# Kernel optimization log

Hardware: AMD Instinct MI355X
Metric: run time of the kernel (lower is better)

Reference implementation:

```python
import jax, jax.numpy as jnp
import numpy as np

H = 128
M = 50000
L = 400000
EPS = 1e-9


def setup_inputs() -> dict:
    key = jax.random.key(0)
    ks = jax.random.split(key, 24)
    d = {
        'x_emb': jax.random.normal(ks[0], (M, H), jnp.float32),
        'child_h': jax.random.normal(ks[1], (M, H), jnp.float32),
        'child_c': jax.random.normal(ks[2], (M, H), jnp.float32),
        'pair_cand_idx': jax.random.randint(ks[3], (L,), 0, M, jnp.int32),
        'pair_child_idx': jax.random.randint(ks[4], (L,), 0, M, jnp.int32),
    }
    s = 1.0 / np.sqrt(H)
    names = ['Wi_w', 'Ui_w', 'Wf_w', 'Uf_w', 'Wo_w', 'Uo_w', 'Wc_w', 'Uc_w', 'Wa_w', 'Ua_w']
    for i, n in enumerate(names):
        d[n] = jax.random.uniform(ks[5 + i], (H, H), jnp.float32, -s, s)
    for i, n in enumerate(['Wi_b', 'Wf_b', 'Wo_b', 'Wc_b', 'Wa_b']):
        d[n] = jax.random.uniform(ks[15 + i], (H,), jnp.float32, -s, s)
    d['v_w'] = jax.random.uniform(ks[20], (H,), jnp.float32, -s, s)
    return d


def reference(x_emb, child_h, child_c, pair_cand_idx, pair_child_idx,
              Wi_w, Ui_w, Wf_w, Uf_w, Wo_w, Uo_w, Wc_w, Uc_w, Wa_w, Ua_w,
              Wi_b, Wf_b, Wo_b, Wc_b, Wa_b, v_w):
    m = x_emb.shape[0]
    ci, chi = pair_cand_idx, pair_child_idx

    # --- segment attention (torch version runs under no_grad) ---
    Ah = child_h @ Wa_w.T + Wa_b          # [M,H]
    Bx = x_emb @ Ua_w.T                   # [M,H]
    e = jnp.tanh(Ah[chi] + Bx[ci]) @ v_w  # [L]
    seg_max = jax.ops.segment_max(e, ci, num_segments=m)
    x_exp = jnp.exp(e - seg_max[ci])
    seg_sum = jax.ops.segment_sum(x_exp, ci, num_segments=m) + EPS
    attn = x_exp / seg_sum[ci]            # [L]
    h_hat = jax.ops.segment_sum(attn[:, None] * child_h[chi], ci, num_segments=m)  # [M,H]

    # --- tree-LSTM gates ---
    i_j = jax.nn.sigmoid(x_emb @ Wi_w.T + Wi_b + h_hat @ Ui_w.T)
    Wfx = x_emb @ Wf_w.T + Wf_b
    Ufh = child_h @ Uf_w.T
    f_pair = jax.nn.sigmoid(Wfx[ci] + Ufh[chi])                       # [L,H]
    sum_f_c = jax.ops.segment_sum(f_pair * child_c[chi], ci, num_segments=m)
    c_t = jnp.tanh(x_emb @ Wc_w.T + Wc_b + h_hat @ Uc_w.T)
    c = i_j * c_t + sum_f_c
    o_j = jax.nn.sigmoid(x_emb @ Wo_w.T + Wo_b + h_hat @ Uo_w.T)
    h = o_j * jnp.tanh(c)
    return (h, c)
```

## Files before the change

### kernel.cpp

```cpp
#include <hip/hip_runtime.h>
#include <cstdint>
#include <cstddef>

#define H 128
#define PSTRIDE 512

typedef __bf16 v8bf __attribute__((ext_vector_type(8)));
typedef __bf16 v4bf __attribute__((ext_vector_type(4)));
typedef float  v4f  __attribute__((ext_vector_type(4)));

__device__ __forceinline__ float ftanh(float x) {
    return 1.f - 2.f / (1.f + __expf(2.f * x));
}
__device__ __forceinline__ float fsigm(float x) {
    return 1.f / (1.f + __expf(-x));
}

struct MatDesc {
    const __bf16* A;
    int           lda;
    const __bf16* Wb;
    const float*  bias;
    __bf16*       C;
    int           ldc;
};
struct MatBatch { MatDesc m[7]; };
struct WPtrs { const float* w[10]; };

__global__ __launch_bounds__(256) void prep_k(WPtrs wp, __bf16* __restrict__ Wb,
                                              const float* __restrict__ x,
                                              const float* __restrict__ chh,
                                              const float* __restrict__ chc,
                                              __bf16* __restrict__ xe,
                                              __bf16* __restrict__ P,
                                              const int* __restrict__ ci,
                                              int* __restrict__ counts,
                                              int MH4, int L) {
    int tid = blockIdx.x * 256 + threadIdx.x;
    if (tid < 40960) {
        int mat = tid >> 12;
        int off = (tid & 4095) << 2;
        v4f a = *(const v4f*)(wp.w[mat] + off);
        v4bf b;
#pragma unroll
        for (int k = 0; k < 4; ++k) b[k] = (__bf16)a[k];
        *(v4bf*)(Wb + mat * 16384 + off) = b;
        return;
    }
    int i = tid - 40960;
    if (i < MH4) {
        v4f a = ((const v4f*)x)[i];
        v4f b = ((const v4f*)chh)[i];
        v4f c = ((const v4f*)chc)[i];
        v4bf ab, bb, cb;
#pragma unroll
        for (int k = 0; k < 4; ++k) {
            ab[k] = (__bf16)a[k]; bb[k] = (__bf16)b[k]; cb[k] = (__bf16)c[k];
        }
        ((v4bf*)xe)[i] = ab;
        int m = i >> 5;
        int q = (i & 31) << 2;
        __bf16* prow = P + (size_t)m * PSTRIDE + q;
        *(v4bf*)prow = bb;
        *(v4bf*)(prow + H) = cb;
        return;
    }
    int l = i - MH4;
    if (l < L) atomicAdd(&counts[ci[l]], 1);
}

__global__ __launch_bounds__(256) void gemm_batch(MatBatch batch, int M) {
    const MatDesc d = batch.m[blockIdx.y];
    __shared__ __bf16 wlds[H][H + 8];

    for (int t = threadIdx.x; t < 2048; t += 256) {
        int n = t >> 4;
        int k = (t & 15) << 3;
        *(v8bf*)&wlds[n][k] = *(const v8bf*)(d.Wb + n * H + k);
    }
    __syncthreads();

    const int wave = threadIdx.x >> 6;
    const int lane = threadIdx.x & 63;
    const int quad = lane >> 4;
    const int l16  = lane & 15;
    const int r0   = blockIdx.x * 128 + wave * 32;

    v4f acc0[8], acc1[8];
#pragma unroll
    for (int nt = 0; nt < 8; ++nt) {
        acc0[nt] = (v4f){0.f, 0.f, 0.f, 0.f};
        acc1[nt] = (v4f){0.f, 0.f, 0.f, 0.f};
    }

    const __bf16* ar0 = d.A + (size_t)(r0 + l16) * d.lda + quad * 8;
    const __bf16* ar1 = d.A + (size_t)(r0 + 16 + l16) * d.lda + quad * 8;
#pragma unroll
    for (int k0 = 0; k0 < H; k0 += 32) {
        v8bf a0 = *(const v8bf*)(ar0 + k0);
        v8bf a1 = *(const v8bf*)(ar1 + k0);
#pragma unroll
        for (int nt = 0; nt < 8; ++nt) {
            v8bf b = *(const v8bf*)(&wlds[nt * 16 + l16][k0 + quad * 8]);
            acc0[nt] = __builtin_amdgcn_mfma_f32_16x16x32_bf16(a0, b, acc0[nt], 0, 0, 0);
            acc1[nt] = __builtin_amdgcn_mfma_f32_16x16x32_bf16(a1, b, acc1[nt], 0, 0, 0);
        }
    }

#pragma unroll
    for (int nt = 0; nt < 8; ++nt) {
        int n = nt * 16 + l16;
        float bia = d.bias ? d.bias[n] : 0.f;
#pragma unroll
        for (int r = 0; r < 4; ++r) {
            int m0 = r0 + quad * 4 + r;
            int m1 = m0 + 16;
            if (m0 < M) d.C[(size_t)m0 * d.ldc + n] = (__bf16)(acc0[nt][r] + bia);
            if (m1 < M) d.C[(size_t)m1 * d.ldc + n] = (__bf16)(acc1[nt][r] + bia);
        }
    }
}

__global__ __launch_bounds__(1024) void scan_local(const int* __restrict__ counts,
                                                   int* __restrict__ excl,
                                                   int* __restrict__ bsums, int M) {
    __shared__ int s[1024];
    int tid = threadIdx.x;
    int idx = blockIdx.x * 1024 + tid;
    int v = (idx < M) ? counts[idx] : 0;
    s[tid] = v;
    __syncthreads();
    for (int off = 1; off < 1024; off <<= 1) {
        int t = (tid >= off) ? s[tid - off] : 0;
        __syncthreads();
        s[tid] += t;
        __syncthreads();
    }
    if (idx < M) excl[idx] = s[tid] - v;
    if (tid == 1023) bsums[blockIdx.x] = s[1023];
}

__global__ __launch_bounds__(1024) void scan_fused(int* __restrict__ rowptr,
                                                   int* __restrict__ cursor,
                                                   const int* __restrict__ bsums,
                                                   const int* __restrict__ counts,
                                                   int M, int nb) {
    __shared__ int s[1024];
    int t = threadIdx.x, b = blockIdx.x;
    int v = (t < nb) ? bsums[t] : 0;
    s[t] = v;
    __syncthreads();
    for (int off = 1; off < 1024; off <<= 1) {
        int tt = (t >= off) ? s[t - off] : 0;
        __syncthreads();
        s[t] += tt;
        __syncthreads();
    }
    int boff = (b == 0) ? 0 : s[b - 1];
    int idx = b * 1024 + t;
    if (idx < M) {
        int val = rowptr[idx] + boff;
        rowptr[idx] = val;
        cursor[idx] = val;
        if (idx == M - 1) rowptr[M] = val + counts[M - 1];
    }
}

__global__ __launch_bounds__(256) void scatter_k(const int* __restrict__ ci,
                                                 const int* __restrict__ chi,
                                                 int* __restrict__ cursor,
                                                 int* __restrict__ payload, int L) {
    int l = blockIdx.x * 256 + threadIdx.x;
    if (l < L) {
        int pos = atomicAdd(&cursor[ci[l]], 1);
        payload[pos] = chi[l];
    }
}

__global__ __launch_bounds__(128) void segment_fused(const int* __restrict__ rowptr,
                                                     const int* __restrict__ payload,
                                                     const float* __restrict__ vw,
                                                     const __bf16* __restrict__ Bx,
                                                     const __bf16* __restrict__ Wfx,
                                                     const __bf16* __restrict__ P,
                                                     __bf16* __restrict__ hhat,
                                                     float* __restrict__ sumfc, int M) {
    const int wl   = threadIdx.x & 63;
    const int half = wl & 32;
    const int l32  = wl & 31;
    const int m = blockIdx.x * 4 + (threadIdx.x >> 5);
    if (m >= M) return;
    const int start = rowptr[m];
    const int deg   = rowptr[m + 1] - start;
    const int h = l32 << 2;

    v4bf bx4 = *(const v4bf*)(Bx + (size_t)m * H + h);
    v4bf wf4 = *(const v4bf*)(Wfx + (size_t)m * H + h);
    v4f  vv  = *(const v4f*)(vw + h);
    float bxf[4], wff[4];
#pragma unroll
    for (int k = 0; k < 4; ++k) { bxf[k] = (float)bx4[k]; wff[k] = (float)wf4[k]; }

    int pl0 = (l32 < deg) ? payload[start + l32] : 0;
    int pl1 = (32 + l32 < deg) ? payload[start + 32 + l32] : 0;

    float denom = 0.f;
    float acch[4] = {0.f, 0.f, 0.f, 0.f};
    float accf[4] = {0.f, 0.f, 0.f, 0.f};

    const int jcap = deg < 64 ? deg : 64;
    for (int j = 0; j < jcap; ++j) {
        int cj = __shfl((j & 32) ? pl1 : pl0, half | (j & 31), 64);
        const __bf16* pb = P + (size_t)cj * PSTRIDE + h;
        v4bf h4 = *(const v4bf*)pb;
        v4bf c4 = *(const v4bf*)(pb + H);
        v4bf u4 = *(const v4bf*)(pb + 2 * H);
        v4bf a4 = *(const v4bf*)(pb + 3 * H);
        float s = 0.f;
#pragma unroll
        for (int k = 0; k < 4; ++k) s += ftanh((float)a4[k] + bxf[k]) * vv[k];
        s += __shfl_xor(s, 1);
        s += __shfl_xor(s, 2);
        s += __shfl_xor(s, 4);
        s += __shfl_xor(s, 8);
        s += __shfl_xor(s, 16);
        float ex = __expf(s);
        denom += ex;
#pragma unroll
        for (int k = 0; k < 4; ++k) {
            acch[k] += ex * (float)h4[k];
            accf[k] += fsigm(wff[k] + (float)u4[k]) * (float)c4[k];
        }
    }
    for (int j = 64; j < deg; ++j) {
        int cj = payload[start + j];
        const __bf16* pb = P + (size_t)cj * PSTRIDE + h;
        v4bf h4 = *(const v4bf*)pb;
        v4bf c4 = *(const v4bf*)(pb + H);
        v4bf u4 = *(const v4bf*)(pb + 2 * H);
        v4bf a4 = *(const v4bf*)(pb + 3 * H);
        float s = 0.f;
#pragma unroll
        for (int k = 0; k < 4; ++k) s += ftanh((float)a4[k] + bxf[k]) * vv[k];
        s += __shfl_xor(s, 1);
        s += __shfl_xor(s, 2);
        s += __shfl_xor(s, 4);
        s += __shfl_xor(s, 8);
        s += __shfl_xor(s, 16);
        float ex = __expf(s);
        denom += ex;
#pragma unroll
        for (int k = 0; k < 4; ++k) {
            acch[k] += ex * (float)h4[k];
            accf[k] += fsigm(wff[k] + (float)u4[k]) * (float)c4[k];
        }
    }

    float inv = 1.f / (denom + 1e-9f);
    v4bf hb;
    v4f sf;
#pragma unroll
    for (int k = 0; k < 4; ++k) { hb[k] = (__bf16)(acch[k] * inv); sf[k] = accf[k]; }
    *(v4bf*)(hhat + (size_t)m * H + h) = hb;
    *(v4f*)(sumfc + (size_t)m * H + h) = sf;
}

__global__ __launch_bounds__(256) void final_k(const __bf16* __restrict__ Xi, const __bf16* __restrict__ Hi,
                                               const __bf16* __restrict__ Xc, const __bf16* __restrict__ Hc,
                                               const __bf16* __restrict__ Xo, const __bf16* __restrict__ Ho,
                                               const float* __restrict__ sumfc,
                                               float* __restrict__ out, int MH4, int MH) {
    int i = blockIdx.x * 256 + threadIdx.x;
    if (i >= MH4) return;
    v4bf xi = ((const v4bf*)Xi)[i], hi = ((const v4bf*)Hi)[i];
    v4bf xc = ((const v4bf*)Xc)[i], hc = ((const v4bf*)Hc)[i];
    v4bf xo = ((const v4bf*)Xo)[i], ho = ((const v4bf*)Ho)[i];
    v4f sf = ((const v4f*)sumfc)[i];
    v4f hout, cout;
#pragma unroll
    for (int k = 0; k < 4; ++k) {
        float ig = fsigm((float)xi[k] + (float)hi[k]);
        float ct = ftanh((float)xc[k] + (float)hc[k]);
        float og = fsigm((float)xo[k] + (float)ho[k]);
        float c = ig * ct + sf[k];
        cout[k] = c;
        hout[k] = og * ftanh(c);
    }
    ((v4f*)out)[i] = hout;
    ((v4f*)(out + MH))[i] = cout;
}

extern "C" void kernel_launch(void* const* d_in, const int* in_sizes, int n_in,
                              void* d_out, int out_size, void* d_ws, size_t ws_size,
                              hipStream_t stream) {
    const float* x_emb   = (const float*)d_in[0];
    const float* child_h = (const float*)d_in[1];
    const float* child_c = (const float*)d_in[2];
    const int*   ci      = (const int*)d_in[3];
    const int*   chi     = (const int*)d_in[4];
    const float* Wi_b = (const float*)d_in[15];
    const float* Wf_b = (const float*)d_in[16];
    const float* Wo_b = (const float*)d_in[17];
    const float* Wc_b = (const float*)d_in[18];
    const float* Wa_b = (const float*)d_in[19];
    const float* vw   = (const float*)d_in[20];

    const int M    = in_sizes[0] / H;
    const int L    = in_sizes[3];
    const int Mpad = (M + 127) & ~127;
    const int MH   = M * H;
    const int MH4  = MH / 4;

    char* p = (char*)d_ws;
    auto alloc = [&](size_t bytes) {
        char* r = p;
        p += (bytes + 255) & ~(size_t)255;
        return (void*)r;
    };
    size_t bfbytes = (size_t)Mpad * H * sizeof(__bf16);
    __bf16* xe16   = (__bf16*)alloc(bfbytes);
    __bf16* P      = (__bf16*)alloc((size_t)Mpad * PSTRIDE * sizeof(__bf16));
    __bf16* hhat16 = (__bf16*)alloc(bfbytes);
    __bf16* Bx16   = (__bf16*)alloc(bfbytes);
    __bf16* Wfx16  = (__bf16*)alloc(bfbytes);
    __bf16* Xi16   = (__bf16*)alloc(bfbytes);
    __bf16* Xc16   = (__bf16*)alloc(bfbytes);
    __bf16* Xo16   = (__bf16*)alloc(bfbytes);
    __bf16* Wb     = (__bf16*)alloc(10 * 16384 * sizeof(__bf16));
    float* sumfc   = (float*)alloc((size_t)MH * 4);
    int*   payload = (int*)alloc((size_t)L * 4);
    int*   counts  = (int*)alloc((size_t)M * 4);
    int*   rowptr  = (int*)alloc((size_t)(M + 1) * 4);
    int*   cursor  = (int*)alloc((size_t)M * 4);
    int*   bsums   = (int*)alloc(1024 * 4);
    __bf16* Hi16 = Bx16;
    __bf16* Hc16 = Wfx16;
    __bf16* Ho16 = P;

    hipMemsetAsync(counts, 0, (size_t)M * 4, stream);

    WPtrs wp;
    for (int k = 0; k < 10; ++k) wp.w[k] = (const float*)d_in[5 + k];
    int prep_items = 40960 + MH4 + L;
    prep_k<<<(prep_items + 255) / 256, 256, 0, stream>>>(wp, Wb, x_emb, child_h, child_c,
                                                         xe16, P, ci, counts, MH4, L);

    const __bf16* Wi = Wb + 0 * 16384;
    const __bf16* Ui = Wb + 1 * 16384;
    const __bf16* Wf = Wb + 2 * 16384;
    const __bf16* Uf = Wb + 3 * 16384;
    const __bf16* Wo = Wb + 4 * 16384;
    const __bf16* Uo = Wb + 5 * 16384;
    const __bf16* Wc = Wb + 6 * 16384;
    const __bf16* Uc = Wb + 7 * 16384;
    const __bf16* Wa = Wb + 8 * 16384;
    const __bf16* Ua = Wb + 9 * 16384;

    MatBatch ba{};
    ba.m[0] = MatDesc{P,    PSTRIDE, Wa, Wa_b,    P + 3 * H, PSTRIDE};
    ba.m[1] = MatDesc{xe16, H,       Ua, nullptr, Bx16,      H};
    ba.m[2] = MatDesc{xe16, H,       Wf, Wf_b,    Wfx16,     H};
    ba.m[3] = MatDesc{P,    PSTRIDE, Uf, nullptr, P + 2 * H, PSTRIDE};
    ba.m[4] = MatDesc{xe16, H,       Wi, Wi_b,    Xi16,      H};
    ba.m[5] = MatDesc{xe16, H,       Wc, Wc_b,    Xc16,      H};
    ba.m[6] = MatDesc{xe16, H,       Wo, Wo_b,    Xo16,      H};
    dim3 gA(Mpad / 128, 7);
    gemm_batch<<<gA, 256, 0, stream>>>(ba, M);

    int nb = (M + 1023) / 1024;
    scan_local<<<nb, 1024, 0, stream>>>(counts, rowptr, bsums, M);
    scan_fused<<<nb, 1024, 0, stream>>>(rowptr, cursor, bsums, counts, M, nb);

    scatter_k<<<(L + 255) / 256, 256, 0, stream>>>(ci, chi, cursor, payload, L);

    segment_fused<<<(M + 3) / 4, 128, 0, stream>>>(rowptr, payload, vw, Bx16, Wfx16, P,
                                                   hhat16, sumfc, M);

    MatBatch bb{};
    bb.m[0] = MatDesc{hhat16, H, Ui, nullptr, Hi16, H};
    bb.m[1] = MatDesc{hhat16, H, Uc, nullptr, Hc16, H};
    bb.m[2] = MatDesc{hhat16, H, Uo, nullptr, Ho16, H};
    dim3 gB(Mpad / 128, 3);
    gemm_batch<<<gB, 256, 0, stream>>>(bb, M);

    final_k<<<(MH4 + 255) / 256, 256, 0, stream>>>(Xi16, Hi16, Xc16, Hc16, Xo16, Ho16, sumfc,
                                                   (float*)d_out, MH4, MH);
}
```

Measured before the change: 397.9 us.

## Fuse GEMMs by shared input, precompute edge scores, fuse final GEMM with gates

The x_emb GEMMs now run as one multi-stage block that converts fp32 rows to bf16 in registers once and reuses them across five weight matrices. The same kernel handles the two P-based GEMMs, and the separate bf16 copy of x_emb is dropped. A new per-edge kernel computes the exp attention scores, scatter carries them into CSR order, and the segment kernel no longer does tanh and reductions per edge. The U-projections of h_hat are fused with the gate epilogue, removing intermediate bf16 buffers and a separate elementwise pass. The costs are extra L-sized buffers, serial weight reloads with more block syncs, and a softmax that skips max subtraction.

Measured after the change: 479.5 us. +20.5%, slower.

```diff
diff --git a/kernel.cpp b/kernel.cpp
--- a/kernel.cpp
+++ b/kernel.cpp
@@ -16,22 +16,14 @@
     return 1.f / (1.f + __expf(-x));
 }
 
-struct MatDesc {
-    const __bf16* A;
-    int           lda;
-    const __bf16* Wb;
-    const float*  bias;
-    __bf16*       C;
-    int           ldc;
-};
-struct MatBatch { MatDesc m[7]; };
+struct Stage { const __bf16* W; const float* bias; __bf16* C; int ldc; };
+struct MultiDesc { const void* A; int lda; int af32; int ns; Stage st[5]; };
+struct MultiBatch { MultiDesc g[2]; };
 struct WPtrs { const float* w[10]; };
 
 __global__ __launch_bounds__(256) void prep_k(WPtrs wp, __bf16* __restrict__ Wb,
-                                              const float* __restrict__ x,
                                               const float* __restrict__ chh,
                                               const float* __restrict__ chc,
-                                              __bf16* __restrict__ xe,
                                               __bf16* __restrict__ P,
                                               const int* __restrict__ ci,
                                               int* __restrict__ counts,
@@ -49,15 +41,11 @@
     }
     int i = tid - 40960;
     if (i < MH4) {
-        v4f a = ((const v4f*)x)[i];
         v4f b = ((const v4f*)chh)[i];
         v4f c = ((const v4f*)chc)[i];
-        v4bf ab, bb, cb;
-#pragma unroll
-        for (int k = 0; k < 4; ++k) {
-            ab[k] = (__bf16)a[k]; bb[k] = (__bf16)b[k]; cb[k] = (__bf16)c[k];
-        }
-        ((v4bf*)xe)[i] = ab;
+        v4bf bb, cb;
+#pragma unroll
+        for (int k = 0; k < 4; ++k) { bb[k] = (__bf16)b[k]; cb[k] = (__bf16)c[k]; }
         int m = i >> 5;
         int q = (i & 31) << 2;
         __bf16* prow = P + (size_t)m * PSTRIDE + q;
@@ -69,16 +57,9 @@
     if (l < L) atomicAdd(&counts[ci[l]], 1);
 }
 
-__global__ __launch_bounds__(256) void gemm_batch(MatBatch batch, int M) {
-    const MatDesc d = batch.m[blockIdx.y];
+__global__ __launch_bounds__(256) void gemm_multi(MultiBatch mb, int M) {
+    const MultiDesc d = mb.g[blockIdx.y];
     __shared__ __bf16 wlds[H][H + 8];
-
-    for (int t = threadIdx.x; t < 2048; t += 256) {
-        int n = t >> 4;
-        int k = (t & 15) << 3;
-        *(v8bf*)&wlds[n][k] = *(const v8bf*)(d.Wb + n * H + k);
-    }
-    __syncthreads();
 
     const int wave = threadIdx.x >> 6;
     const int lane = threadIdx.x & 63;
@@ -86,39 +67,108 @@
     const int l16  = lane & 15;
     const int r0   = blockIdx.x * 128 + wave * 32;
 
-    v4f acc0[8], acc1[8];
-#pragma unroll
-    for (int nt = 0; nt < 8; ++nt) {
-        acc0[nt] = (v4f){0.f, 0.f, 0.f, 0.f};
-        acc1[nt] = (v4f){0.f, 0.f, 0.f, 0.f};
-    }
-
-    const __bf16* ar0 = d.A + (size_t)(r0 + l16) * d.lda + quad * 8;
-    const __bf16* ar1 = d.A + (size_t)(r0 + 16 + l16) * d.lda + quad * 8;
-#pragma unroll
-    for (int k0 = 0; k0 < H; k0 += 32) {
-        v8bf a0 = *(const v8bf*)(ar0 + k0);
-        v8bf a1 = *(const v8bf*)(ar1 + k0);
+    int ra = r0 + l16;      if (ra > M - 1) ra = M - 1;
+    int rb = r0 + 16 + l16; if (rb > M - 1) rb = M - 1;
+
+    v8bf a0[4], a1[4];
+    if (d.af32) {
+        const float* A = (const float*)d.A;
+        const float* p0 = A + (size_t)ra * d.lda + quad * 8;
+        const float* p1 = A + (size_t)rb * d.lda + quad * 8;
+#pragma unroll
+        for (int k0 = 0; k0 < 4; ++k0) {
+            v4f x0a = *(const v4f*)(p0 + k0 * 32);
+            v4f x0b = *(const v4f*)(p0 + k0 * 32 + 4);
+            v4f x1a = *(const v4f*)(p1 + k0 * 32);
+            v4f x1b = *(const v4f*)(p1 + k0 * 32 + 4);
+            v8bf t0, t1;
+#pragma unroll
+            for (int k = 0; k < 4; ++k) {
+                t0[k] = (__bf16)x0a[k]; t0[k + 4] = (__bf16)x0b[k];
+                t1[k] = (__bf16)x1a[k]; t1[k + 4] = (__bf16)x1b[k];
+            }
+            a0[k0] = t0; a1[k0] = t1;
+        }
+    } else {
+        const __bf16* A = (const __bf16*)d.A;
+        const __bf16* p0 = A + (size_t)ra * d.lda + quad * 8;
+        const __bf16* p1 = A + (size_t)rb * d.lda + quad * 8;
+#pragma unroll
+        for (int k0 = 0; k0 < 4; ++k0) {
+            a0[k0] = *(const v8bf*)(p0 + k0 * 32);
+            a1[k0] = *(const v8bf*)(p1 + k0 * 32);
+        }
+    }
+
+    for (int s = 0; s < d.ns; ++s) {
+        if (s) __syncthreads();
+        for (int t = threadIdx.x; t < 2048; t += 256) {
+            int n = t >> 4;
+            int k = (t & 15) << 3;
+            *(v8bf*)&wlds[n][k] = *(const v8bf*)(d.st[s].W + n * H + k);
+        }
+        __syncthreads();
+
+        v4f acc0[8], acc1[8];
 #pragma unroll
         for (int nt = 0; nt < 8; ++nt) {
-            v8bf b = *(const v8bf*)(&wlds[nt * 16 + l16][k0 + quad * 8]);
-            acc0[nt] = __builtin_amdgcn_mfma_f32_16x16x32_bf16(a0, b, acc0[nt], 0, 0, 0);
-            acc1[nt] = __builtin_amdgcn_mfma_f32_16x16x32_bf16(a1, b, acc1[nt], 0, 0, 0);
-        }
-    }
-
-#pragma unroll
-    for (int nt = 0; nt < 8; ++nt) {
-        int n = nt * 16 + l16;
-        float bia = d.bias ? d.bias[n] : 0.f;
-#pragma unroll
-        for (int r = 0; r < 4; ++r) {
-            int m0 = r0 + quad * 4 + r;
-            int m1 = m0 + 16;
-            if (m0 < M) d.C[(size_t)m0 * d.ldc + n] = (__bf16)(acc0[nt][r] + bia);
-            if (m1 < M) d.C[(size_t)m1 * d.ldc + n] = (__bf16)(acc1[nt][r] + bia);
-        }
-    }
+            acc0[nt] = (v4f){0.f, 0.f, 0.f, 0.f};
+            acc1[nt] = (v4f){0.f, 0.f, 0.f, 0.f};
+        }
+#pragma unroll
+        for (int k0 = 0; k0 < 4; ++k0) {
+#pragma unroll
+            for (int nt = 0; nt < 8; ++nt) {
+                v8bf b = *(const v8bf*)(&wlds[nt * 16 + l16][k0 * 32 + quad * 8]);
+                acc0[nt] = __builtin_amdgcn_mfma_f32_16x16x32_bf16(a0[k0], b, acc0[nt], 0, 0, 0);
+                acc1[nt] = __builtin_amdgcn_mfma_f32_16x16x32_bf16(a1[k0], b, acc1[nt], 0, 0, 0);
+            }
+        }
+
+        const float* bias = d.st[s].bias;
+        __bf16* C = d.st[s].C;
+        const int ldc = d.st[s].ldc;
+#pragma unroll
+        for (int nt = 0; nt < 8; ++nt) {
+            int n = nt * 16 + l16;
+            float bia = bias ? bias[n] : 0.f;
+#pragma unroll
+            for (int r = 0; r < 4; ++r) {
+                int m0 = r0 + quad * 4 + r;
+                int m1 = m0 + 16;
+                if (m0 < M) C[(size_t)m0 * ldc + n] = (__bf16)(acc0[nt][r] + bia);
+                if (m1 < M) C[(size_t)m1 * ldc + n] = (__bf16)(acc1[nt][r] + bia);
+            }
+        }
+    }
+}
+
+__global__ __launch_bounds__(256) void edge_score(const int* __restrict__ ci,
+                                                  const int* __restrict__ chi,
+                                                  const float* __restrict__ vw,
+                                                  const __bf16* __restrict__ Bx,
+                                                  const __bf16* __restrict__ P,
+                                                  float* __restrict__ ex_out, int L) {
+    int e = blockIdx.x * 8 + (threadIdx.x >> 5);
+    if (e >= L) return;
+    const int l32 = threadIdx.x & 31;
+    const int h = l32 << 2;
+    int m  = ci[e];
+    int cj = chi[e];
+
+    v4bf a4 = *(const v4bf*)(P + (cj << 9) + 3 * H + h);
+    v4bf b4 = *(const v4bf*)(Bx + (m << 7) + h);
+    v4f  vv = *(const v4f*)(vw + h);
+
+    float s = 0.f;
+#pragma unroll
+    for (int k = 0; k < 4; ++k) s += ftanh((float)a4[k] + (float)b4[k]) * vv[k];
+    s += __shfl_xor(s, 1);
+    s += __shfl_xor(s, 2);
+    s += __shfl_xor(s, 4);
+    s += __shfl_xor(s, 8);
+    s += __shfl_xor(s, 16);
+    if (l32 == 0) ex_out[e] = __expf(s);
 }
 
 __global__ __launch_bounds__(1024) void scan_local(const int* __restrict__ counts,
@@ -168,19 +218,23 @@
 
 __global__ __launch_bounds__(256) void scatter_k(const int* __restrict__ ci,
                                                  const int* __restrict__ chi,
+                                                 const float* __restrict__ ex_e,
                                                  int* __restrict__ cursor,
-                                                 int* __restrict__ payload, int L) {
+                                                 int* __restrict__ payload,
+                                                 float* __restrict__ exs, int L) {
     int l = blockIdx.x * 256 + threadIdx.x;
     if (l < L) {
+        float ex = ex_e[l];
+        int c = chi[l];
         int pos = atomicAdd(&cursor[ci[l]], 1);
-        payload[pos] = chi[l];
-    }
-}
-
-__global__ __launch_bounds__(128) void segment_fused(const int* __restrict__ rowptr,
+        payload[pos] = c;
+        exs[pos] = ex;
+    }
+}
+
+__global__ __launch_bounds__(256) void segment_fused(const int* __restrict__ rowptr,
                                                      const int* __restrict__ payload,
-                                                     const float* __restrict__ vw,
-                                                     const __bf16* __restrict__ Bx,
+                                                     const float* __restrict__ exs,
                                                      const __bf16* __restrict__ Wfx,
                                                      const __bf16* __restrict__ P,
                                                      __bf16* __restrict__ hhat,
@@ -188,21 +242,21 @@
     const int wl   = threadIdx.x & 63;
     const int half = wl & 32;
     const int l32  = wl & 31;
-    const int m = blockIdx.x * 4 + (threadIdx.x >> 5);
+    const int m = blockIdx.x * 8 + (threadIdx.x >> 5);
     if (m >= M) return;
     const int start = rowptr[m];
     const int deg   = rowptr[m + 1] - start;
     const int h = l32 << 2;
 
-    v4bf bx4 = *(const v4bf*)(Bx + (size_t)m * H + h);
-    v4bf wf4 = *(const v4bf*)(Wfx + (size_t)m * H + h);
-    v4f  vv  = *(const v4f*)(vw + h);
-    float bxf[4], wff[4];
-#pragma unroll
-    for (int k = 0; k < 4; ++k) { bxf[k] = (float)bx4[k]; wff[k] = (float)wf4[k]; }
-
-    int pl0 = (l32 < deg) ? payload[start + l32] : 0;
-    int pl1 = (32 + l32 < deg) ? payload[start + 32 + l32] : 0;
+    v4bf wf4 = *(const v4bf*)(Wfx + (m << 7) + h);
+    float wff[4];
+#pragma unroll
+    for (int k = 0; k < 4; ++k) wff[k] = (float)wf4[k];
+
+    int   pl0 = (l32 < deg) ? payload[start + l32] : 0;
+    int   pl1 = (32 + l32 < deg) ? payload[start + 32 + l32] : 0;
+    float ex0 = (l32 < deg) ? exs[start + l32] : 0.f;
+    float ex1 = (32 + l32 < deg) ? exs[start + 32 + l32] : 0.f;
 
     float denom = 0.f;
     float acch[4] = {0.f, 0.f, 0.f, 0.f};
@@ -210,48 +264,30 @@
 
     const int jcap = deg < 64 ? deg : 64;
     for (int j = 0; j < jcap; ++j) {
-        int cj = __shfl((j & 32) ? pl1 : pl0, half | (j & 31), 64);
-        const __bf16* pb = P + (size_t)cj * PSTRIDE + h;
-        v4bf h4 = *(const v4bf*)pb;
-        v4bf c4 = *(const v4bf*)(pb + H);
-        v4bf u4 = *(const v4bf*)(pb + 2 * H);
-        v4bf a4 = *(const v4bf*)(pb + 3 * H);
-        float s = 0.f;
-#pragma unroll
-        for (int k = 0; k < 4; ++k) s += ftanh((float)a4[k] + bxf[k]) * vv[k];
-        s += __shfl_xor(s, 1);
-        s += __shfl_xor(s, 2);
-        s += __shfl_xor(s, 4);
-        s += __shfl_xor(s, 8);
-        s += __shfl_xor(s, 16);
-        float ex = __expf(s);
+        int   cj = __shfl((j & 32) ? pl1 : pl0, half | (j & 31), 64);
+        float ex = __shfl((j & 32) ? ex1 : ex0, half | (j & 31), 64);
+        int off = (cj << 9) + h;
+        v4bf h4 = *(const v4bf*)(P + off);
+        v4bf c4 = *(const v4bf*)(P + off + H);
+        v4bf u4 = *(const v4bf*)(P + off + 2 * H);
         denom += ex;
 #pragma unroll
         for (int k = 0; k < 4; ++k) {
-            acch[k] += ex * (float)h4[k];
+            acch[k] = fmaf(ex, (float)h4[k], acch[k]);
             accf[k] += fsigm(wff[k] + (float)u4[k]) * (float)c4[k];
         }
     }
     for (int j = 64; j < deg; ++j) {
-        int cj = payload[start + j];
-        const __bf16* pb = P + (size_t)cj * PSTRIDE + h;
-        v4bf h4 = *(const v4bf*)pb;
-        v4bf c4 = *(const v4bf*)(pb + H);
-        v4bf u4 = *(const v4bf*)(pb + 2 * H);
-        v4bf a4 = *(const v4bf*)(pb + 3 * H);
-        float s = 0.f;
-#pragma unroll
-        for (int k = 0; k < 4; ++k) s += ftanh((float)a4[k] + bxf[k]) * vv[k];
-        s += __shfl_xor(s, 1);
-        s += __shfl_xor(s, 2);
-        s += __shfl_xor(s, 4);
-        s += __shfl_xor(s, 8);
-        s += __shfl_xor(s, 16);
-        float ex = __expf(s);
+        int   cj = payload[start + j];
+        float ex = exs[start + j];
+        int off = (cj << 9) + h;
+        v4bf h4 = *(const v4bf*)(P + off);
+        v4bf c4 = *(const v4bf*)(P + off + H);
+        v4bf u4 = *(const v4bf*)(P + off + 2 * H);
         denom += ex;
 #pragma unroll
         for (int k = 0; k < 4; ++k) {
-            acch[k] += ex * (float)h4[k];
+            acch[k] = fmaf(ex, (float)h4[k], acch[k]);
             accf[k] += fsigm(wff[k] + (float)u4[k]) * (float)c4[k];
         }
     }
@@ -265,29 +301,82 @@
     *(v4f*)(sumfc + (size_t)m * H + h) = sf;
 }
 
-__global__ __launch_bounds__(256) void final_k(const __bf16* __restrict__ Xi, const __bf16* __restrict__ Hi,
-                                               const __bf16* __restrict__ Xc, const __bf16* __restrict__ Hc,
-                                               const __bf16* __restrict__ Xo, const __bf16* __restrict__ Ho,
-                                               const float* __restrict__ sumfc,
-                                               float* __restrict__ out, int MH4, int MH) {
-    int i = blockIdx.x * 256 + threadIdx.x;
-    if (i >= MH4) return;
-    v4bf xi = ((const v4bf*)Xi)[i], hi = ((const v4bf*)Hi)[i];
-    v4bf xc = ((const v4bf*)Xc)[i], hc = ((const v4bf*)Hc)[i];
-    v4bf xo = ((const v4bf*)Xo)[i], ho = ((const v4bf*)Ho)[i];
-    v4f sf = ((const v4f*)sumfc)[i];
-    v4f hout, cout;
-#pragma unroll
-    for (int k = 0; k < 4; ++k) {
-        float ig = fsigm((float)xi[k] + (float)hi[k]);
-        float ct = ftanh((float)xc[k] + (float)hc[k]);
-        float og = fsigm((float)xo[k] + (float)ho[k]);
-        float c = ig * ct + sf[k];
-        cout[k] = c;
-        hout[k] = og * ftanh(c);
-    }
-    ((v4f*)out)[i] = hout;
-    ((v4f*)(out + MH))[i] = cout;
+__global__ __launch_bounds__(256) void gemm_final(const __bf16* __restrict__ hhat,
+                                                  const __bf16* __restrict__ Ui,
+                                                  const __bf16* __restrict__ Uc,
+                                                  const __bf16* __restrict__ Uo,
+                                                  const __bf16* __restrict__ Xi,
+                                                  const __bf16* __restrict__ Xc,
+                                                  const __bf16* __restrict__ Xo,
+                                                  const float* __restrict__ sumfc,
+                                                  float* __restrict__ out, int M, int MH) {
+    __shared__ __bf16 wl[3][H][H + 8];
+
+    for (int t = threadIdx.x; t < 6144; t += 256) {
+        int w = t >> 11;
+        int n = (t >> 4) & 127;
+        int k = (t & 15) << 3;
+        const __bf16* src = (w == 0) ? Ui : (w == 1) ? Uc : Uo;
+        *(v8bf*)&wl[w][n][k] = *(const v8bf*)(src + n * H + k);
+    }
+    __syncthreads();
+
+    const int wave = threadIdx.x >> 6;
+    const int lane = threadIdx.x & 63;
+    const int quad = lane >> 4;
+    const int l16  = lane & 15;
+    const int r0   = blockIdx.x * 128 + wave * 32;
+
+    const __bf16* p0 = hhat + (size_t)(r0 + l16) * H + quad * 8;
+    const __bf16* p1 = hhat + (size_t)(r0 + 16 + l16) * H + quad * 8;
+    v8bf a0[4], a1[4];
+#pragma unroll
+    for (int k0 = 0; k0 < 4; ++k0) {
+        a0[k0] = *(const v8bf*)(p0 + k0 * 32);
+        a1[k0] = *(const v8bf*)(p1 + k0 * 32);
+    }
+
+#pragma unroll
+    for (int nt = 0; nt < 8; ++nt) {
+        v4f ai0 = (v4f){0.f, 0.f, 0.f, 0.f}, ai1 = ai0;
+        v4f ac0 = ai0, ac1 = ai0, ao0 = ai0, ao1 = ai0;
+#pragma unroll
+        for (int k0 = 0; k0 < 4; ++k0) {
+            v8bf bi = *(const v8bf*)(&wl[0][nt * 16 + l16][k0 * 32 + quad * 8]);
+            v8bf bc = *(const v8bf*)(&wl[1][nt * 16 + l16][k0 * 32 + quad * 8]);
+            v8bf bo = *(const v8bf*)(&wl[2][nt * 16 + l16][k0 * 32 + quad * 8]);
+            ai0 = __builtin_amdgcn_mfma_f32_16x16x32_bf16(a0[k0], bi, ai0, 0, 0, 0);
+            ai1 = __builtin_amdgcn_mfma_f32_16x16x32_bf16(a1[k0], bi, ai1, 0, 0, 0);
+            ac0 = __builtin_amdgcn_mfma_f32_16x16x32_bf16(a0[k0], bc, ac0, 0, 0, 0);
+            ac1 = __builtin_amdgcn_mfma_f32_16x16x32_bf16(a1[k0], bc, ac1, 0, 0, 0);
+            ao0 = __builtin_amdgcn_mfma_f32_16x16x32_bf16(a0[k0], bo, ao0, 0, 0, 0);
+            ao1 = __builtin_amdgcn_mfma_f32_16x16x32_bf16(a1[k0], bo, ao1, 0, 0, 0);
+        }
+        int n = nt * 16 + l16;
+#pragma unroll
+        for (int r = 0; r < 4; ++r) {
+            int m0 = r0 + quad * 4 + r;
+            if (m0 < M) {
+                size_t idx = (size_t)m0 * H + n;
+                float ig = fsigm((float)Xi[idx] + ai0[r]);
+                float ct = ftanh((float)Xc[idx] + ac0[r]);
+                float og = fsigm((float)Xo[idx] + ao0[r]);
+                float c = ig * ct + sumfc[idx];
+                out[idx] = og * ftanh(c);
+                out[MH + idx] = c;
+            }
+            int m1 = m0 + 16;
+            if (m1 < M) {
+                size_t idx = (size_t)m1 * H + n;
+                float ig = fsigm((float)Xi[idx] + ai1[r]);
+                float ct = ftanh((float)Xc[idx] + ac1[r]);
+                float og = fsigm((float)Xo[idx] + ao1[r]);
+                float c = ig * ct + sumfc[idx];
+                out[idx] = og * ftanh(c);
+                out[MH + idx] = c;
+            }
+        }
+    }
 }
 
 extern "C" void kernel_launch(void* const* d_in, const int* in_sizes, int n_in,
@@ -318,7 +407,6 @@
         return (void*)r;
     };
     size_t bfbytes = (size_t)Mpad * H * sizeof(__bf16);
-    __bf16* xe16   = (__bf16*)alloc(bfbytes);
     __bf16* P      = (__bf16*)alloc((size_t)Mpad * PSTRIDE * sizeof(__bf16));
     __bf16* hhat16 = (__bf16*)alloc(bfbytes);
     __bf16* Bx16   = (__bf16*)alloc(bfbytes);
@@ -328,22 +416,21 @@
     __bf16* Xo16   = (__bf16*)alloc(bfbytes);
     __bf16* Wb     = (__bf16*)alloc(10 * 16384 * sizeof(__bf16));
     float* sumfc   = (float*)alloc((size_t)MH * 4);
+    float* ex_e    = (float*)alloc((size_t)L * 4);
+    float* exs     = (float*)alloc((size_t)L * 4);
     int*   payload = (int*)alloc((size_t)L * 4);
     int*   counts  = (int*)alloc((size_t)M * 4);
     int*   rowptr  = (int*)alloc((size_t)(M + 1) * 4);
     int*   cursor  = (int*)alloc((size_t)M * 4);
     int*   bsums   = (int*)alloc(1024 * 4);
-    __bf16* Hi16 = Bx16;
-    __bf16* Hc16 = Wfx16;
-    __bf16* Ho16 = P;
 
     hipMemsetAsync(counts, 0, (size_t)M * 4, stream);
 
     WPtrs wp;
     for (int k = 0; k < 10; ++k) wp.w[k] = (const float*)d_in[5 + k];
     int prep_items = 40960 + MH4 + L;
-    prep_k<<<(prep_items + 255) / 256, 256, 0, stream>>>(wp, Wb, x_emb, child_h, child_c,
-                                                         xe16, P, ci, counts, MH4, L);
+    prep_k<<<(prep_items + 255) / 256, 256, 0, stream>>>(wp, Wb, child_h, child_c,
+                                                         P, ci, counts, MH4, L);
 
     const __bf16* Wi = Wb + 0 * 16384;
     const __bf16* Ui = Wb + 1 * 16384;
@@ -356,33 +443,29 @@
     const __bf16* Wa = Wb + 8 * 16384;
     const __bf16* Ua = Wb + 9 * 16384;
 
-    MatBatch ba{};
-    ba.m[0] = MatDesc{P,    PSTRIDE, Wa, Wa_b,    P + 3 * H, PSTRIDE};
-    ba.m[1] = MatDesc{xe16, H,       Ua, nullptr, Bx16,      H};
-    ba.m[2] = MatDesc{xe16, H,       Wf, Wf_b,    Wfx16,     H};
-    ba.m[3] = MatDesc{P,    PSTRIDE, Uf, nullptr, P + 2 * H, PSTRIDE};
-    ba.m[4] = MatDesc{xe16, H,       Wi, Wi_b,    Xi16,      H};
-    ba.m[5] = MatDesc{xe16, H,       Wc, Wc_b,    Xc16,      H};
-    ba.m[6] = MatDesc{xe16, H,       Wo, Wo_b,    Xo16,      H};
-    dim3 gA(Mpad / 128, 7);
-    gemm_batch<<<gA, 256, 0, stream>>>(ba, M);
+    MultiBatch mb{};
+    mb.g[0].A = x_emb; mb.g[0].lda = H; mb.g[0].af32 = 1; mb.g[0].ns = 5;
+    mb.g[0].st[0] = Stage{Ua, nullptr, Bx16, H};
+    mb.g[0].st[1] = Stage{Wf, Wf_b, Wfx16, H};
+    mb.g[0].st[2] = Stage{Wi, Wi_b, Xi16, H};
+    mb.g[0].st[3] = Stage{Wc, Wc_b, Xc16, H};
+    mb.g[0].st[4] = Stage{Wo, Wo_b, Xo16, H};
+    mb.g[1].A = P; mb.g[1].lda = PSTRIDE; mb.g[1].af32 = 0; mb.g[1].ns = 2;
+    mb.g[1].st[0] = Stage{Wa, Wa_b, P + 3 * H, PSTRIDE};
+    mb.g[1].st[1] = Stage{Uf, nullptr, P + 2 * H, PSTRIDE};
+    gemm_multi<<<dim3(Mpad / 128, 2), 256, 0, stream>>>(mb, M);
+
+    edge_score<<<(L + 7) / 8, 256, 0, stream>>>(ci, chi, vw, Bx16, P, ex_e, L);
 
     int nb = (M + 1023) / 1024;
     scan_local<<<nb, 1024, 0, stream>>>(counts, rowptr, bsums, M);
     scan_fused<<<nb, 1024, 0, stream>>>(rowptr, cursor, bsums, counts, M, nb);
 
-    scatter_k<<<(L + 255) / 256, 256, 0, stream>>>(ci, chi, cursor, payload, L);
-
-    segment_fused<<<(M + 3) / 4, 128, 0, stream>>>(rowptr, payload, vw, Bx16, Wfx16, P,
+    scatter_k<<<(L + 255) / 256, 256, 0, stream>>>(ci, chi, ex_e, cursor, payload, exs, L);
+
+    segment_fused<<<(M + 7) / 8, 256, 0, stream>>>(rowptr, payload, exs, Wfx16, P,
                                                    hhat16, sumfc, M);
 
-    MatBatch bb{};
-    bb.m[0] = MatDesc{hhat16, H, Ui, nullptr, Hi16, H};
-    bb.m[1] = MatDesc{hhat16, H, Uc, nullptr, Hc16, H};
-    bb.m[2] = MatDesc{hhat16, H, Uo, nullptr, Ho16, H};
-    dim3 gB(Mpad / 128, 3);
-    gemm_batch<<<gB, 256, 0, stream>>>(bb, M);
-
-    final_k<<<(MH4 + 255) / 256, 256, 0, stream>>>(Xi16, Hi16, Xc16, Hc16, Xo16, Ho16, sumfc,
-                                                   (float*)d_out, MH4, MH);
-}
+    gemm_final<<<Mpad / 128, 256, 0, stream>>>(hhat16, Ui, Uc, Uo, Xi16, Xc16, Xo16,
+                                               sumfc, (float*)d_out, M, MH);
+}
```
